# Kernel tuning notes

Measured on AMD Instinct MI355X. Metric: run time of the kernel, lower is better.

The kernel has to match this reference:

```python
import jax, jax.numpy as jnp
import numpy as np

B, L, D, H, NL, EXP = 8, 1024, 512, 8, 6, 4
DH = D // H
DF = D * EXP
EPS = 1e-3  # keras LayerNormalization default epsilon
NEG = -1e9  # keras Softmax mask adder for float32


def _ln(x, g, b):
    m = jnp.mean(x, axis=-1, keepdims=True)
    v = jnp.mean(jnp.square(x - m), axis=-1, keepdims=True)
    return (x - m) * jax.lax.rsqrt(v + EPS) * g + b


def _pos_emb(L, D):
    pos = jnp.arange(L, dtype=jnp.float32)[:, None]          # [L,1]
    i = jnp.arange(D // 2, dtype=jnp.float32)[None, :]        # [1,D/2]
    inv = jnp.power(10000.0, -2.0 * i / D)
    # original concatenates sin block then cos block along feature axis
    return jnp.concatenate([jnp.sin(pos * inv), jnp.cos(pos * inv)], axis=-1)  # [L,D]


def setup_inputs() -> dict:
    key = jax.random.key(0)
    ks = jax.random.split(key, 16)
    glorot = lambda k, shape: jax.random.uniform(
        k, shape, jnp.float32, -1.0, 1.0) * jnp.sqrt(6.0 / (shape[-2] + shape[-1]))
    return {
        "x": jax.random.normal(ks[0], (B, L, D), jnp.float32),
        "lengths": jax.random.randint(ks[1], (B,), L // 2, L + 1).astype(jnp.int32),
        "Wq": glorot(ks[2], (NL, D, D)),
        "Wk": glorot(ks[3], (NL, D, D)),
        "Wv": glorot(ks[4], (NL, D, D)),
        "Wo": glorot(ks[5], (NL, D, D)),
        "ln1_g": jnp.ones((NL, D), jnp.float32),
        "ln1_b": jnp.zeros((NL, D), jnp.float32),
        "ln2_g": jnp.ones((NL, D), jnp.float32),
        "ln2_b": jnp.zeros((NL, D), jnp.float32),
        "w1": glorot(ks[6], (NL, D, DF)),
        "b1": jnp.zeros((NL, DF), jnp.float32),
        "w2": glorot(ks[7], (NL, DF, D)),
        "b2": jnp.zeros((NL, D), jnp.float32),
    }


def _forward(x, mask_bias, Wq, Wk, Wv, Wo, ln1_g, ln1_b, ln2_g, ln2_b, w1, b1, w2, b2):
    x = x + _pos_emb(L, D)[None, :, :]
    scale = 1.0 / jnp.sqrt(jnp.float32(DH))

    def layer(x, p):
        wq, wk, wv, wo, g1, be1, g2, be2, fw1, fb1, fw2, fb2 = p
        h = _ln(x, g1, be1)
        split = lambda t: t.reshape(B, L, H, DH).transpose(0, 2, 1, 3)  # [B,H,L,DH]
        q, k, v = split(h @ wq), split(h @ wk), split(h @ wv)
        scores = jnp.einsum("bhqd,bhkd->bhqk", q, k) * scale + mask_bias
        attn = jax.nn.softmax(scores, axis=-1)
        o = jnp.einsum("bhqk,bhkd->bhqd", attn, v)
        o = o.transpose(0, 2, 1, 3).reshape(B, L, D) @ wo
        x = x + o  # dropout is identity at inference
        h2 = _ln(x, g2, be2)
        ffn = jax.nn.relu(h2 @ fw1 + fb1) @ fw2 + fb2
        return x + ffn, None

    x, _ = jax.lax.scan(layer, x, (Wq, Wk, Wv, Wo, ln1_g, ln1_b, ln2_g, ln2_b, w1, b1, w2, b2))
    return x


def reference(x, lengths, Wq, Wk, Wv, Wo, ln1_g, ln1_b, ln2_g, ln2_b, w1, b1, w2, b2):
    mask = (jnp.arange(L)[None, :] < lengths[:, None]).astype(jnp.float32)  # [B,L]
    mask_bias = (1.0 - mask)[:, None, None, :] * NEG                        # [B,1,1,L]
    return _forward(x, mask_bias, Wq, Wk, Wv, Wo, ln1_g, ln1_b, ln2_g, ln2_b, w1, b1, w2, b2)
```

## Files before the change

### kernel.cpp

```cpp
#include <hip/hip_runtime.h>
#include <cstdint>
#include <cstddef>

#define Bz 8
#define Lz 1024
#define Dz 512
#define Hz 8
#define NLz 6
#define DFz 2048
#define Mz (Bz*Lz)

typedef short bf16x8 __attribute__((ext_vector_type(8)));
typedef float f32x4  __attribute__((ext_vector_type(4)));

__device__ __forceinline__ short f2bf(float f) {
    unsigned u = __builtin_bit_cast(unsigned, f);
    u = (u + 0x7fff + ((u >> 16) & 1)) >> 16;
    return (short)u;
}

__device__ __forceinline__ float exp2_fast(float x) {
#if __has_builtin(__builtin_amdgcn_exp2f)
    return __builtin_amdgcn_exp2f(x);
#else
    return exp2f(x);
#endif
}

#define GLD16(gp, lp) __builtin_amdgcn_global_load_lds( \
    (const __attribute__((address_space(1))) void*)(gp), \
    (__attribute__((address_space(3))) void*)(lp), 16, 0, 0)

__global__ __launch_bounds__(256) void posadd_kernel(const float* __restrict__ x,
                                                     float* __restrict__ y) {
    int idx = blockIdx.x * 256 + threadIdx.x;
    int d   = idx & (Dz - 1);
    int pos = (idx >> 9) & (Lz - 1);
    int i2  = (d < Dz/2) ? d : d - Dz/2;
    float inv = __expf(-0.03597789207f * (float)i2);
    float a = (float)pos * inv;
    float pe = (d < Dz/2) ? sinf(a) : cosf(a);
    y[idx] = x[idx] + pe;
}

__global__ __launch_bounds__(256) void ln_kernel(const float* __restrict__ x,
                                                 const float* __restrict__ g,
                                                 const float* __restrict__ b,
                                                 short* __restrict__ out) {
    int row = blockIdx.x;
    int t = threadIdx.x;
    const float* xr = x + (size_t)row * Dz;
    float v0 = xr[t], v1 = xr[t + 256];
    float s = v0 + v1;
    #pragma unroll
    for (int off = 32; off; off >>= 1) s += __shfl_xor(s, off, 64);
    __shared__ float red[4];
    int w = t >> 6, l = t & 63;
    if (l == 0) red[w] = s;
    __syncthreads();
    float m = (red[0] + red[1] + red[2] + red[3]) * (1.0f / Dz);
    float d0 = v0 - m, d1 = v1 - m;
    float s2 = d0 * d0 + d1 * d1;
    #pragma unroll
    for (int off = 32; off; off >>= 1) s2 += __shfl_xor(s2, off, 64);
    __syncthreads();
    if (l == 0) red[w] = s2;
    __syncthreads();
    float var = (red[0] + red[1] + red[2] + red[3]) * (1.0f / Dz);
    float rs = rsqrtf(var + 1e-3f);
    out[(size_t)row * Dz + t]       = f2bf(d0 * rs * g[t] + b[t]);
    out[(size_t)row * Dz + t + 256] = f2bf(d1 * rs * g[t + 256] + b[t + 256]);
}

__global__ __launch_bounds__(256) void transpose_bf16_kernel(const float* __restrict__ src,
                                                             short* __restrict__ dst,
                                                             int K, int N,
                                                             long srcLS, long dstLS, int rowOff) {
    __shared__ float tile[32][33];
    int tx = threadIdx.x & 31, ty = threadIdx.x >> 5;
    int bx = blockIdx.x, by = blockIdx.y, z = blockIdx.z;
    const float* s = src + (size_t)z * srcLS;
    short* d = dst + (size_t)z * dstLS;
    #pragma unroll
    for (int i = 0; i < 4; i++)
        tile[ty + i * 8][tx] = s[(size_t)(by * 32 + ty + i * 8) * N + bx * 32 + tx];
    __syncthreads();
    #pragma unroll
    for (int i = 0; i < 4; i++)
        d[(size_t)(rowOff + bx * 32 + ty + i * 8) * K + by * 32 + tx] = f2bf(tile[tx][ty + i * 8]);
}

__global__ __launch_bounds__(256) void vtrans_kernel(const short* __restrict__ qkv,
                                                     short* __restrict__ vbt) {
    int lt = blockIdx.x, bh = blockIdx.y;
    int b = bh >> 3, h = bh & 7;
    __shared__ short tile[64][72];
    int t = threadIdx.x;
    int l = t >> 2, c4 = t & 3;
    #pragma unroll
    for (int p = 0; p < 2; p++) {
        int dd = (c4 + p * 4) * 8;
        *(uint4*)&tile[l][dd] =
            *(const uint4*)(qkv + ((size_t)(b * Lz + lt * 64 + l)) * 1536 + 1024 + h * 64 + dd);
    }
    __syncthreads();
    int d = t >> 2;
    #pragma unroll
    for (int p = 0; p < 2; p++) {
        int lc = (c4 + p * 4) * 8;
        union { uint4 u; short s[8]; } o;
        #pragma unroll
        for (int j = 0; j < 8; j++) o.s[j] = tile[lc + j][d];
        *(uint4*)(vbt + ((size_t)(bh * 64 + d)) * Lz + lt * 64 + lc) = o.u;
    }
}

template<int MODE, int TN>
__global__ __launch_bounds__(256, (TN == 64) ? 4 : 2)
void gemm_bt(const short* __restrict__ A,
             const short* __restrict__ Bt,
             short* __restrict__ outb,
             float* __restrict__ outf,
             const float* __restrict__ bias,
             int M, int N, int K) {
    constexpr int NI = TN / 32;
    __shared__ __attribute__((aligned(16))) short As[128 * 32];
    __shared__ __attribute__((aligned(16))) short Bs[TN * 32];
    int t = threadIdx.x;
    int m0 = blockIdx.x * 128, n0 = blockIdx.y * TN;
    int w = t >> 6, l = t & 63;
    int wm = (w >> 1) * 64, wn = (w & 1) * (TN / 2);
    int lr = l & 15, lq = l >> 4;
    f32x4 acc[4][NI] = {};
    int ra0 = t >> 2, ca0 = (t & 3) * 8;
    int ra1 = (t + 256) >> 2;
    for (int kk = 0; kk < K; kk += 32) {
        GLD16(A + (size_t)(m0 + ra0) * K + kk + ca0, As + t * 8);
        GLD16(A + (size_t)(m0 + ra1) * K + kk + ca0, As + (t + 256) * 8);
        GLD16(Bt + (size_t)(n0 + ra0) * K + kk + ca0, Bs + t * 8);
        if constexpr (TN == 128)
            GLD16(Bt + (size_t)(n0 + ra1) * K + kk + ca0, Bs + (t + 256) * 8);
        __syncthreads();
        bf16x8 af[4], bfr[NI];
        #pragma unroll
        for (int i = 0; i < 4; i++)  af[i]  = *(const bf16x8*)(As + (wm + i * 16 + lr) * 32 + lq * 8);
        #pragma unroll
        for (int i = 0; i < NI; i++) bfr[i] = *(const bf16x8*)(Bs + (wn + i * 16 + lr) * 32 + lq * 8);
        #pragma unroll
        for (int mi = 0; mi < 4; mi++)
            #pragma unroll
            for (int ni = 0; ni < NI; ni++)
                acc[mi][ni] = __builtin_amdgcn_mfma_f32_16x16x32_bf16(af[mi], bfr[ni], acc[mi][ni], 0, 0, 0);
        __syncthreads();
    }
    #pragma unroll
    for (int mi = 0; mi < 4; mi++)
        #pragma unroll
        for (int ni = 0; ni < NI; ni++) {
            int col = n0 + wn + ni * 16 + lr;
            float bv = (MODE == 2 || MODE == 3) ? bias[col] : 0.0f;
            #pragma unroll
            for (int r = 0; r < 4; r++) {
                int row = m0 + wm + mi * 16 + lq * 4 + r;
                size_t idx = (size_t)row * N + col;
                float v = acc[mi][ni][r];
                if (MODE == 0)      outb[idx] = f2bf(v);
                else if (MODE == 1) outf[idx] += v;
                else if (MODE == 2) outb[idx] = f2bf(fmaxf(v + bv, 0.0f));
                else                outf[idx] += v + bv;
            }
        }
}

__device__ __forceinline__ void attn_frag(f32x4* sacc, const float* biask,
                                          float* mr, float* lsum, f32x4* oacc,
                                          short* Pw, const short* Vs,
                                          int lr, int lq, bf16x8 onesf) {
    const float SC2 = 0.18033688f;
    float p[8][4];
    #pragma unroll
    for (int r = 0; r < 4; r++) {
        float mx = -1e30f;
        #pragma unroll
        for (int kt = 0; kt < 8; kt++) {
            p[kt][r] = sacc[kt][r] * SC2 + biask[kt];
            mx = fmaxf(mx, p[kt][r]);
        }
        mx = fmaxf(mx, __shfl_xor(mx, 1, 64));
        mx = fmaxf(mx, __shfl_xor(mx, 2, 64));
        mx = fmaxf(mx, __shfl_xor(mx, 4, 64));
        mx = fmaxf(mx, __shfl_xor(mx, 8, 64));
        float mn = fmaxf(mr[r], mx);
        float alpha = exp2_fast(mr[r] - mn);
        mr[r] = mn;
        #pragma unroll
        for (int kt = 0; kt < 8; kt++)
            p[kt][r] = exp2_fast(p[kt][r] - mn);
        lsum[r] *= alpha;
        #pragma unroll
        for (int ni = 0; ni < 4; ni++) oacc[ni][r] *= alpha;
    }
    #pragma unroll
    for (int kt = 0; kt < 8; kt++)
        #pragma unroll
        for (int r = 0; r < 4; r++)
            Pw[(lq * 4 + r) * 136 + kt * 16 + lr] = f2bf(p[kt][r]);
    f32x4 sums = {};
    #pragma unroll
    for (int c = 0; c < 4; c++) {
        bf16x8 pf = *(const bf16x8*)(Pw + lr * 136 + c * 32 + lq * 8);
        sums = __builtin_amdgcn_mfma_f32_16x16x32_bf16(pf, onesf, sums, 0, 0, 0);
        #pragma unroll
        for (int ni = 0; ni < 4; ni++) {
            bf16x8 vf = *(const bf16x8*)(Vs + (ni * 16 + lr) * 136 + c * 32 + lq * 8);
            oacc[ni] = __builtin_amdgcn_mfma_f32_16x16x32_bf16(pf, vf, oacc[ni], 0, 0, 0);
        }
    }
    #pragma unroll
    for (int r = 0; r < 4; r++) lsum[r] += sums[r];
}

__global__ __launch_bounds__(256, 2) void attn_kernel(const short* __restrict__ qkv,
                                                      const short* __restrict__ vbt,
                                                      const int* __restrict__ lengths,
                                                      short* __restrict__ o) {
    __shared__ __attribute__((aligned(16))) short Ks[128 * 72];
    __shared__ __attribute__((aligned(16))) short Vs[64 * 136];
    __shared__ __attribute__((aligned(16))) short Ps[4][16 * 136];
    int qt = blockIdx.y;
    int bh = blockIdx.x;
    int b = bh >> 3, h = bh & 7;
    int len = lengths[b];
    int t = threadIdx.x, w = t >> 6, l = t & 63;
    int lr = l & 15, lq = l >> 4;

    const short* q0 = qkv + (size_t)(b * Lz + qt * 128 + w * 32 + lr) * 1536 + h * 64 + lq * 8;
    bf16x8 qf0a = *(const bf16x8*)(q0);
    bf16x8 qf0b = *(const bf16x8*)(q0 + 32);
    bf16x8 qf1a = *(const bf16x8*)(q0 + 16 * 1536);
    bf16x8 qf1b = *(const bf16x8*)(q0 + 16 * 1536 + 32);

    int kkey = t >> 3, kd8 = (t & 7) * 8;
    int vd = t >> 4, vk8 = (t & 15) * 8;
    const short* kbaseg = qkv + (size_t)(b * Lz) * 1536 + 512 + h * 64;
    const short* vbaseg = vbt + (size_t)(bh * 64) * Lz;

    float mr0[4] = {-1e30f, -1e30f, -1e30f, -1e30f}, ls0[4] = {0.f, 0.f, 0.f, 0.f};
    float mr1[4] = {-1e30f, -1e30f, -1e30f, -1e30f}, ls1[4] = {0.f, 0.f, 0.f, 0.f};
    f32x4 oacc0[4] = {}, oacc1[4] = {};
    bf16x8 onesf = {0x3F80, 0x3F80, 0x3F80, 0x3F80, 0x3F80, 0x3F80, 0x3F80, 0x3F80};

    uint4 kreg[4], vreg[4];
    #pragma unroll
    for (int i = 0; i < 4; i++)
        kreg[i] = *(const uint4*)(kbaseg + (size_t)(i * 32 + kkey) * 1536 + kd8);

    short* Pw = &Ps[w][0];
    int ntiles = (len + 127) >> 7;
    for (int tix = 0; tix < ntiles; tix++) {
        int k0 = tix << 7;
        __syncthreads();
        #pragma unroll
        for (int i = 0; i < 4; i++)
            *(uint4*)(Ks + (i * 32 + kkey) * 72 + kd8) = kreg[i];
        __syncthreads();
        #pragma unroll
        for (int i = 0; i < 4; i++)
            vreg[i] = *(const uint4*)(vbaseg + (size_t)(i * 16 + vd) * Lz + k0 + vk8);
        f32x4 sacc[8] = {};
        #pragma unroll
        for (int kt = 0; kt < 8; kt++) {
            bf16x8 kf0 = *(const bf16x8*)(Ks + (kt * 16 + lr) * 72 + lq * 8);
            bf16x8 kf1 = *(const bf16x8*)(Ks + (kt * 16 + lr) * 72 + 32 + lq * 8);
            sacc[kt] = __builtin_amdgcn_mfma_f32_16x16x32_bf16(qf0a, kf0, sacc[kt], 0, 0, 0);
            sacc[kt] = __builtin_amdgcn_mfma_f32_16x16x32_bf16(qf0b, kf1, sacc[kt], 0, 0, 0);
        }
        if (tix + 1 < ntiles) {
            #pragma unroll
            for (int i = 0; i < 4; i++)
                kreg[i] = *(const uint4*)(kbaseg + (size_t)(k0 + 128 + i * 32 + kkey) * 1536 + kd8);
        }
        #pragma unroll
        for (int i = 0; i < 4; i++)
            *(uint4*)(Vs + (i * 16 + vd) * 136 + vk8) = vreg[i];
        float biask[8];
        #pragma unroll
        for (int kt = 0; kt < 8; kt++)
            biask[kt] = ((k0 + kt * 16 + lr) < len) ? 0.0f : -1e30f;
        __syncthreads();
        attn_frag(sacc, biask, mr0, ls0, oacc0, Pw, Vs, lr, lq, onesf);
        #pragma unroll
        for (int kt = 0; kt < 8; kt++) {
            bf16x8 kf0 = *(const bf16x8*)(Ks + (kt * 16 + lr) * 72 + lq * 8);
            bf16x8 kf1 = *(const bf16x8*)(Ks + (kt * 16 + lr) * 72 + 32 + lq * 8);
            f32x4 s2 = {};
            s2 = __builtin_amdgcn_mfma_f32_16x16x32_bf16(qf1a, kf0, s2, 0, 0, 0);
            s2 = __builtin_amdgcn_mfma_f32_16x16x32_bf16(qf1b, kf1, s2, 0, 0, 0);
            sacc[kt] = s2;
        }
        attn_frag(sacc, biask, mr1, ls1, oacc1, Pw, Vs, lr, lq, onesf);
    }
    #pragma unroll
    for (int ni = 0; ni < 4; ni++)
        #pragma unroll
        for (int r = 0; r < 4; r++) {
            int q = qt * 128 + w * 32 + lq * 4 + r;
            size_t base = (size_t)(b * Lz + q) * Dz + h * 64 + ni * 16 + lr;
            o[base]             = f2bf(oacc0[ni][r] / ls0[r]);
            o[base + 16 * Dz]   = f2bf(oacc1[ni][r] / ls1[r]);
        }
}

extern "C" void kernel_launch(void* const* d_in, const int* in_sizes, int n_in,
                              void* d_out, int out_size, void* d_ws, size_t ws_size,
                              hipStream_t stream) {
    const float* x_in    = (const float*)d_in[0];
    const int*   lengths = (const int*)d_in[1];
    const float* Wq   = (const float*)d_in[2];
    const float* Wk   = (const float*)d_in[3];
    const float* Wv   = (const float*)d_in[4];
    const float* Wo   = (const float*)d_in[5];
    const float* ln1g = (const float*)d_in[6];
    const float* ln1b = (const float*)d_in[7];
    const float* ln2g = (const float*)d_in[8];
    const float* ln2b = (const float*)d_in[9];
    const float* w1   = (const float*)d_in[10];
    const float* b1   = (const float*)d_in[11];
    const float* w2   = (const float*)d_in[12];
    const float* b2   = (const float*)d_in[13];

    size_t off = 0;
    auto alloc = [&](size_t bytes) {
        void* p = (char*)d_ws + off;
        off += (bytes + 255) & ~(size_t)255;
        return p;
    };
    float* x_work = (float*)alloc((size_t)Mz * Dz * 4);
    short* hbuf   = (short*)alloc((size_t)Mz * Dz * 2);
    short* qkvb   = (short*)alloc((size_t)Mz * 1536 * 2);
    short* f1b    = (short*)alloc((size_t)Mz * DFz * 2);
    short* vbt    = (short*)alloc((size_t)Bz * Hz * 64 * Lz * 2);
    short* wqkvT  = (short*)alloc((size_t)NLz * 1536 * Dz * 2);
    short* woT    = (short*)alloc((size_t)NLz * Dz * Dz * 2);
    short* w1T    = (short*)alloc((size_t)NLz * DFz * Dz * 2);
    short* w2T    = (short*)alloc((size_t)NLz * Dz * DFz * 2);

    dim3 tb(256);
    transpose_bf16_kernel<<<dim3(16, 16, NLz), tb, 0, stream>>>(Wq, wqkvT, Dz, Dz, (long)Dz*Dz, (long)1536*Dz, 0);
    transpose_bf16_kernel<<<dim3(16, 16, NLz), tb, 0, stream>>>(Wk, wqkvT, Dz, Dz, (long)Dz*Dz, (long)1536*Dz, 512);
    transpose_bf16_kernel<<<dim3(16, 16, NLz), tb, 0, stream>>>(Wv, wqkvT, Dz, Dz, (long)Dz*Dz, (long)1536*Dz, 1024);
    transpose_bf16_kernel<<<dim3(16, 16, NLz), tb, 0, stream>>>(Wo, woT, Dz, Dz, (long)Dz*Dz, (long)Dz*Dz, 0);
    transpose_bf16_kernel<<<dim3(64, 16, NLz), tb, 0, stream>>>(w1, w1T, Dz, DFz, (long)Dz*DFz, (long)DFz*Dz, 0);
    transpose_bf16_kernel<<<dim3(16, 64, NLz), tb, 0, stream>>>(w2, w2T, DFz, Dz, (long)DFz*Dz, (long)Dz*DFz, 0);

    posadd_kernel<<<dim3(Mz * Dz / 256), tb, 0, stream>>>(x_in, x_work);

    for (int lyr = 0; lyr < NLz; lyr++) {
        const short* wqkvL = wqkvT + (size_t)lyr * 1536 * Dz;
        const short* woL   = woT   + (size_t)lyr * Dz * Dz;
        const short* w1L   = w1T   + (size_t)lyr * DFz * Dz;
        const short* w2L   = w2T   + (size_t)lyr * Dz * DFz;

        ln_kernel<<<dim3(Mz), tb, 0, stream>>>(x_work, ln1g + lyr * Dz, ln1b + lyr * Dz, hbuf);
        gemm_bt<0,128><<<dim3(Mz/128, 1536/128), tb, 0, stream>>>(hbuf, wqkvL, qkvb, nullptr, nullptr, Mz, 1536, Dz);
        vtrans_kernel<<<dim3(Lz/64, Bz*Hz), tb, 0, stream>>>(qkvb, vbt);
        attn_kernel<<<dim3(Bz*Hz, Lz/128), tb, 0, stream>>>(qkvb, vbt, lengths, hbuf);
        gemm_bt<1,64><<<dim3(Mz/128, Dz/64), tb, 0, stream>>>(hbuf, woL, nullptr, x_work, nullptr, Mz, Dz, Dz);
        ln_kernel<<<dim3(Mz), tb, 0, stream>>>(x_work, ln2g + lyr * Dz, ln2b + lyr * Dz, hbuf);
        gemm_bt<2,128><<<dim3(Mz/128, DFz/128), tb, 0, stream>>>(hbuf, w1L, f1b, nullptr, b1 + lyr * DFz, Mz, DFz, Dz);
        gemm_bt<3,64><<<dim3(Mz/128, Dz/64), tb, 0, stream>>>(f1b, w2L, nullptr, x_work, b2 + lyr * Dz, Mz, Dz, DFz);
    }

    hipMemcpyAsync(d_out, x_work, (size_t)Mz * Dz * 4, hipMemcpyDeviceToDevice, stream);
}
```

Before: 1.186 ms.

## Double GEMM K-step to 64 with XOR-swizzled LDS layout

The bf16 GEMM now stages a K-slice of 64 instead of 32 per iteration, which halves the number of barrier pairs and global-load rounds over K. It also stores the tiles in LDS with an XOR swizzle on the 16-byte column chunk so that the MFMA fragment reads avoid bank conflicts. This doubles the shared-memory footprint and raises register use, and launch bounds are fixed at 2 waves per SIMD for all tile widths. That setting may lower occupancy for the TN=64 variant.

```diff
diff --git a/kernel.cpp b/kernel.cpp
--- a/kernel.cpp
+++ b/kernel.cpp
@@ -116,7 +116,7 @@
 }
 
 template<int MODE, int TN>
-__global__ __launch_bounds__(256, (TN == 64) ? 4 : 2)
+__global__ __launch_bounds__(256, 2)
 void gemm_bt(const short* __restrict__ A,
              const short* __restrict__ Bt,
              short* __restrict__ outb,
@@ -124,33 +124,46 @@
              const float* __restrict__ bias,
              int M, int N, int K) {
     constexpr int NI = TN / 32;
-    __shared__ __attribute__((aligned(16))) short As[128 * 32];
-    __shared__ __attribute__((aligned(16))) short Bs[TN * 32];
+    __shared__ __attribute__((aligned(16))) short As[128 * 64];
+    __shared__ __attribute__((aligned(16))) short Bs[TN * 64];
     int t = threadIdx.x;
     int m0 = blockIdx.x * 128, n0 = blockIdx.y * TN;
     int w = t >> 6, l = t & 63;
     int wm = (w >> 1) * 64, wn = (w & 1) * (TN / 2);
     int lr = l & 15, lq = l >> 4;
     f32x4 acc[4][NI] = {};
-    int ra0 = t >> 2, ca0 = (t & 3) * 8;
-    int ra1 = (t + 256) >> 2;
-    for (int kk = 0; kk < K; kk += 32) {
-        GLD16(A + (size_t)(m0 + ra0) * K + kk + ca0, As + t * 8);
-        GLD16(A + (size_t)(m0 + ra1) * K + kk + ca0, As + (t + 256) * 8);
-        GLD16(Bt + (size_t)(n0 + ra0) * K + kk + ca0, Bs + t * 8);
-        if constexpr (TN == 128)
-            GLD16(Bt + (size_t)(n0 + ra1) * K + kk + ca0, Bs + (t + 256) * 8);
-        __syncthreads();
-        bf16x8 af[4], bfr[NI];
-        #pragma unroll
-        for (int i = 0; i < 4; i++)  af[i]  = *(const bf16x8*)(As + (wm + i * 16 + lr) * 32 + lq * 8);
-        #pragma unroll
-        for (int i = 0; i < NI; i++) bfr[i] = *(const bf16x8*)(Bs + (wn + i * 16 + lr) * 32 + lq * 8);
+    int sr = t >> 3;
+    int sc = ((t & 7) ^ (sr & 7)) * 8;
+    for (int kk = 0; kk < K; kk += 64) {
+        #pragma unroll
+        for (int i = 0; i < 4; i++)
+            GLD16(A + (size_t)(m0 + sr + i * 32) * K + kk + sc, As + i * 2048 + t * 8);
+        #pragma unroll
+        for (int i = 0; i < TN / 32; i++)
+            GLD16(Bt + (size_t)(n0 + sr + i * 32) * K + kk + sc, Bs + i * 2048 + t * 8);
+        __syncthreads();
+        bf16x8 af[4][2], bfr[NI][2];
+        #pragma unroll
+        for (int i = 0; i < 4; i++) {
+            int row = wm + i * 16 + lr;
+            const short* rp = As + row * 64;
+            af[i][0] = *(const bf16x8*)(rp + ((lq ^ (row & 7)) * 8));
+            af[i][1] = *(const bf16x8*)(rp + (((4 + lq) ^ (row & 7)) * 8));
+        }
+        #pragma unroll
+        for (int i = 0; i < NI; i++) {
+            int row = wn + i * 16 + lr;
+            const short* rp = Bs + row * 64;
+            bfr[i][0] = *(const bf16x8*)(rp + ((lq ^ (row & 7)) * 8));
+            bfr[i][1] = *(const bf16x8*)(rp + (((4 + lq) ^ (row & 7)) * 8));
+        }
         #pragma unroll
         for (int mi = 0; mi < 4; mi++)
             #pragma unroll
-            for (int ni = 0; ni < NI; ni++)
-                acc[mi][ni] = __builtin_amdgcn_mfma_f32_16x16x32_bf16(af[mi], bfr[ni], acc[mi][ni], 0, 0, 0);
+            for (int ni = 0; ni < NI; ni++) {
+                acc[mi][ni] = __builtin_amdgcn_mfma_f32_16x16x32_bf16(af[mi][0], bfr[ni][0], acc[mi][ni], 0, 0, 0);
+                acc[mi][ni] = __builtin_amdgcn_mfma_f32_16x16x32_bf16(af[mi][1], bfr[ni][1], acc[mi][ni], 0, 0, 0);
+            }
         __syncthreads();
     }
     #pragma unroll
```

Measured after the change: 1.087 ms. 1.09x faster.
